# Kernel tuning notes

Measured on AMD Instinct MI355X. Metric: run time of the kernel, lower is better.

Reference implementation:

```python
import jax, jax.numpy as jnp
import numpy as np

B, D, H = 4096, 64, 1024  # batch, state dim, hidden width


def setup_inputs() -> dict:
    key = jax.random.key(0)
    ks = jax.random.split(key, 4)
    def w(k, shape, fan_in):
        return (jax.random.normal(k, shape, jnp.float32) / np.float32(np.sqrt(fan_in)))
    return {
        "x": jax.random.normal(ks[0], (B, 1 + D), jnp.float32),
        "W1": w(ks[1], (D, H), D),
        "b1": jnp.zeros((H,), jnp.float32),
        "W2": w(ks[2], (H, H), H),
        "b2": jnp.zeros((H,), jnp.float32),
        "W3": w(ks[3], (H, D), H),
        "b3": jnp.zeros((D,), jnp.float32),
    }


def _mlp(z, W1, b1, W2, b2, W3, b3):
    # tanh MLP vector field: d -> h -> h -> d
    h = jnp.tanh(z @ W1 + b1)
    h = jnp.tanh(h @ W2 + b2)
    return h @ W3 + b3


def reference(x, W1, b1, W2, b2, W3, b3):
    x_in = x[:, 1:]                        # [B, D] state (col 0 is logp channel)
    f = lambda z: _mlp(z, W1, b1, W2, b2, W3, b3)
    x_out = f(x_in)                        # [B, D]

    # Exact Jacobian trace: same math as the torch per-dim autograd.grad loop,
    # expressed as D forward-mode JVPs vmapped over the identity basis.
    eye = jnp.eye(x_in.shape[1], dtype=x.dtype)

    def diag_entry(e):                     # e: [D] basis vector
        _, t = jax.jvp(f, (x_in,), (jnp.broadcast_to(e, x_in.shape),))
        return t @ e                       # [B] = J[:, i, i]

    trJ = jnp.sum(jax.vmap(diag_entry)(eye), axis=0)  # [B]

    out = jnp.concatenate([-trJ[:, None], x_out], axis=1)  # [B, 1+D]
    return out + 0.0 * x  # faithful to `+ 0 * x` in the original
```

## Files before the change

kernel.cpp:

```cpp
#include <hip/hip_runtime.h>
#include <cmath>

typedef unsigned short u16;
typedef __attribute__((ext_vector_type(8))) short s8v;
typedef __attribute__((ext_vector_type(4))) float f4v;
typedef __attribute__((ext_vector_type(16))) float f16v;

__device__ __forceinline__ u16 f2bf(float f) {
    union { float f; unsigned u; } v; v.f = f;
    unsigned r = v.u + 0x7FFFu + ((v.u >> 16) & 1u);
    return (u16)(r >> 16);
}
__device__ __forceinline__ float tanh_fast(float x) {
    float e = __builtin_amdgcn_exp2f(x * 2.88539008177792681f);
    return 1.f - 2.f * __builtin_amdgcn_rcpf(1.f + e);
}
__device__ __forceinline__ int wslot(int row, int c) {
    return ((((c >> 2) << 6) | ((c & 3) << 4) | (row & 15)) ^ c);
}
__device__ __forceinline__ size_t fragoff(int n, int k) {
    return (((size_t)(n >> 5) * 64 + (k >> 4)) * 64 + (n & 31) + (((k >> 3) & 1) << 5)) * 8 + (k & 7);
}

__launch_bounds__(256)
__global__ void cnf_prep(const float* __restrict__ x, const float* __restrict__ W1,
                         const float* __restrict__ W2, const float* __restrict__ W3,
                         u16* __restrict__ W2Tf, u16* __restrict__ VTf,
                         u16* __restrict__ xb, u16* __restrict__ W1T,
                         u16* __restrict__ W3Tf, float* __restrict__ trJ)
{
    __shared__ float w2s[32][33];
    __shared__ __align__(16) float w1s[64][36];
    const int a = blockIdx.x * 32;
    const int b = blockIdx.y * 32;
    const int t = threadIdx.x;

    #pragma unroll
    for (int it = 0; it < 4; ++it) {
        int idx = t + it * 256;
        w2s[idx >> 5][idx & 31] = W2[(a + (idx >> 5)) * 1024 + b + (idx & 31)];
    }
    #pragma unroll
    for (int it = 0; it < 8; ++it) {
        int idx = t + it * 256;
        w1s[idx >> 5][idx & 31] = W1[(idx >> 5) * 1024 + a + (idx & 31)];
    }
    __syncthreads();

    #pragma unroll
    for (int it = 0; it < 4; ++it) {
        int idx = t + it * 256;
        int rr = idx >> 5, cc = idx & 31;
        W2Tf[fragoff(b + rr, a + cc)] = f2bf(w2s[cc][rr]);
    }
    {
        const int q = t >> 3, pg = t & 7;
        const float* w3row = W3 + (b + q) * 64;
        f4v u = f4v{0.f, 0.f, 0.f, 0.f};
        #pragma unroll
        for (int i4 = 0; i4 < 16; ++i4) {
            f4v w3v = *(const f4v*)&w3row[i4 * 4];
            #pragma unroll
            for (int s = 0; s < 4; ++s) {
                f4v wv = *(const f4v*)&w1s[i4 * 4 + s][pg * 4];
                u += w3v[s] * wv;
            }
        }
        #pragma unroll
        for (int j = 0; j < 4; ++j) {
            const int pp = pg * 4 + j;
            VTf[fragoff(b + q, a + pp)] = f2bf(w2s[pp][q] * u[j]);
        }
    }
    {
        int bid = blockIdx.y * 32 + blockIdx.x;
        int e = bid * 256 + t;
        xb[e] = f2bf(x[(e >> 6) * 65 + 1 + (e & 63)]);
    }
    if (blockIdx.y == 0) {
        int pp = t >> 3, i0 = (t & 7) * 8;
        s8v v;
        #pragma unroll
        for (int j = 0; j < 8; ++j) v[j] = (short)f2bf(w1s[i0 + j][pp]);
        *(s8v*)&W1T[(a + pp) * 64 + i0] = v;
        if (t < 128) trJ[blockIdx.x * 128 + t] = 0.f;
    }
    if (blockIdx.y == 1) {
        int idx = blockIdx.x * 256 + t;
        int n = idx & 63, k0 = (idx >> 6) * 8;
        s8v v;
        #pragma unroll
        for (int j = 0; j < 8; ++j) v[j] = (short)f2bf(W3[(k0 + j) * 64 + n]);
        *(s8v*)&W3Tf[fragoff(n, k0)] = v;
    }
}

__launch_bounds__(256)
__global__ void cnf_gemm1(const u16* __restrict__ xb, const u16* __restrict__ W1T,
                          const float* __restrict__ b1,
                          u16* __restrict__ h1f, u16* __restrict__ g1f)
{
    __shared__ __align__(16) u16 lds[12 * 1024];
    __shared__ __align__(16) u16 hls[128 * 64];
    __shared__ __align__(16) u16 gls[128 * 64];
    const int t = threadIdx.x;
    const int wave = t >> 6, lane = t & 63;
    const int wm = wave >> 1, wn = wave & 1;
    const int g = lane >> 4, lr = lane & 15;
    const int arow0 = blockIdx.x * 128, bcol0 = blockIdx.y * 64;

    #pragma unroll
    for (int i = 0; i < 4; ++i) {
        int ch = t + i * 256, row = ch >> 3, c = ch & 7;
        *(s8v*)&lds[(row >> 4) * 1024 + wslot(row, c) * 8] =
            *(const s8v*)&xb[(arow0 + row) * 64 + c * 8];
    }
    #pragma unroll
    for (int i = 0; i < 2; ++i) {
        int ch = t + i * 256, row = ch >> 3, c = ch & 7;
        *(s8v*)&lds[(8 + (row >> 4)) * 1024 + wslot(row, c) * 8] =
            *(const s8v*)&W1T[(bcol0 + row) * 64 + c * 8];
    }
    __syncthreads();

    f4v acc[4][2];
    #pragma unroll
    for (int mi = 0; mi < 4; ++mi)
        #pragma unroll
        for (int ni = 0; ni < 2; ++ni) acc[mi][ni] = f4v{0.f,0.f,0.f,0.f};

    #pragma unroll
    for (int ks = 0; ks < 2; ++ks) {
        const int lo = (ks * 64 + (lane ^ ((ks * 4 + g) & 7))) * 8;
        s8v af[4], bf[2];
        #pragma unroll
        for (int mi = 0; mi < 4; ++mi) af[mi] = *(const s8v*)&lds[(wm * 4 + mi) * 1024 + lo];
        #pragma unroll
        for (int ni = 0; ni < 2; ++ni) bf[ni] = *(const s8v*)&lds[(8 + wn * 2 + ni) * 1024 + lo];
        #pragma unroll
        for (int mi = 0; mi < 4; ++mi)
            #pragma unroll
            for (int ni = 0; ni < 2; ++ni)
                acc[mi][ni] = __builtin_amdgcn_mfma_f32_16x16x32_bf16(af[mi], bf[ni], acc[mi][ni], 0, 0, 0);
    }

    #pragma unroll
    for (int mi = 0; mi < 4; ++mi) {
        const int rowl = wm * 64 + mi * 16 + g * 4;
        #pragma unroll
        for (int ni = 0; ni < 2; ++ni) {
            const int coll = wn * 32 + ni * 16 + lr;
            const float bv = b1[bcol0 + coll];
            const int cc = coll >> 3, jj = coll & 7;
            #pragma unroll
            for (int r = 0; r < 4; ++r) {
                const int row = rowl + r;
                float h = tanh_fast(acc[mi][ni][r] + bv);
                int idx = row * 64 + ((cc ^ (row & 7)) << 3) + jj;
                hls[idx] = f2bf(h);
                gls[idx] = f2bf(1.f - h * h);
            }
        }
    }
    __syncthreads();

    const int rt0 = arow0 >> 5, kk0 = bcol0 >> 4;
    #pragma unroll
    for (int i = 0; i < 4; ++i) {
        const int tile = (i * 256 + t) >> 6;
        const int ln = t & 63;
        const int rt = tile >> 2, kk = tile & 3;
        const int row = rt * 32 + (ln & 31);
        const int kb = kk * 16 + (ln >> 5) * 8;
        const int src = row * 64 + (((kb >> 3) ^ (row & 7)) << 3);
        const size_t dst = ((size_t)(rt0 + rt) * 64 + (kk0 + kk)) * 512 + ln * 8;
        *(s8v*)&h1f[dst] = *(const s8v*)&hls[src];
        *(s8v*)&g1f[dst] = *(const s8v*)&gls[src];
    }
}

#define LOADB(B, kt)                                                           \
    do { _Pragma("unroll")                                                     \
         for (int _ks = 0; _ks < 2; ++_ks) {                                   \
             size_t _o = (((size_t)(ntb + wn) * 64 + (kt) * 2 + _ks) * 512) + lane * 8; \
             B[_ks*2 + 0] = *(const s8v*)&W2Tf[_o];                            \
             B[_ks*2 + 1] = *(const s8v*)&VTf[_o];                             \
         } } while (0)

#define MIDBODY(kt, AwH, AwG, AlH, AlG, Bc, Bn)                                \
    {                                                                          \
        const u16* _buf = &lds[(kt) & 1][0];                                   \
        s8v a1[2][2], a2[2][2];                                  \
        _Pragma("unroll")                                                      \
        for (int ks = 0; ks < 2; ++ks)                                         \
            _Pragma("unroll")                                                  \
            for (int mt = 0; mt < 2; ++mt) {                                   \
                const int f = ((wrt * 2 + mt) * 2 + ks) * 512 + lane * 8;      \
                a1[ks][mt] = *(const s8v*)&_buf[f];                            \
                a2[ks][mt] = *(const s8v*)&_buf[4096 + f];                     \
            }                                                                  \
        if ((kt) < 30) {                                                       \
            const size_t _go = (size_t)((kt) + 2) * 1024;                      \
            AlH = *(const s8v*)(h1f + sg0 + _go);                              \
            AlG = *(const s8v*)(g1f + sg0 + _go);                              \
        }                                                                      \
        if ((kt) < 31) {                                                       \
            u16* _wb = &lds[((kt) + 1) & 1][0];                                \
            *(s8v*)&_wb[sd0] = AwH; *(s8v*)&_wb[4096 + sd0] = AwG;             \
            LOADB(Bn, (kt) + 1);                                               \
        }                                                                      \
        _Pragma("unroll")                                                      \
        for (int ks = 0; ks < 2; ++ks)                                         \
            _Pragma("unroll")                                                  \
            for (int mt = 0; mt < 2; ++mt) {                                   \
                acc1[mt] = __builtin_amdgcn_mfma_f32_32x32x16_bf16(a1[ks][mt], Bc[ks*2+0], acc1[mt], 0, 0, 0); \
                acc2[mt] = __builtin_amdgcn_mfma_f32_32x32x16_bf16(a2[ks][mt], Bc[ks*2+1], acc2[mt], 0, 0, 0); \
            }                                                                  \
        __syncthreads();                                                       \
    }

__launch_bounds__(512, 1)
__global__ void cnf_mid(const u16* __restrict__ h1f, const u16* __restrict__ g1f,
                        const u16* __restrict__ W2Tf, const u16* __restrict__ VTf,
                        const float* __restrict__ b2,
                        u16* __restrict__ h2f, float* __restrict__ trJ)
{
    __shared__ __align__(16) u16 lds[2][8192];

    const int t = threadIdx.x;
    const int wave = t >> 6, lane = t & 63;
    const int wrt = wave & 1;
    const int wn  = wave >> 1;
    const int bid = blockIdx.x;
    const int k8 = bid & 7, j = bid >> 3;
    const int bx = k8 * 4 + (j & 3);
    const int by = j >> 2;
    const int arow0 = bx * 128;
    const int ntb = by * 4;

    const int lc8 = (t & 63) * 8;
    const int rt_s = t >> 7, kk_s = (t >> 6) & 1;
    const size_t sg0 = ((size_t)(bx * 4 + rt_s) * 64 + kk_s) * 512 + lc8;
    const int sd0 = (rt_s * 2 + kk_s) * 512 + lc8;

    f16v acc1[2], acc2[2];
    #pragma unroll
    for (int mt = 0; mt < 2; ++mt)
        #pragma unroll
        for (int r = 0; r < 16; ++r) { acc1[mt][r] = 0.f; acc2[mt][r] = 0.f; }

    s8v raH, raG, rbH, rbG;
    s8v bA[4], bB[4];

    raH = *(const s8v*)(h1f + sg0);
    raG = *(const s8v*)(g1f + sg0);
    {
        u16* wb = &lds[0][0];
        *(s8v*)&wb[sd0] = raH; *(s8v*)&wb[4096 + sd0] = raG;
    }
    raH = *(const s8v*)(h1f + sg0 + 1024);
    raG = *(const s8v*)(g1f + sg0 + 1024);
    LOADB(bA, 0);
    __syncthreads();

    for (int kt2 = 0; kt2 < 16; ++kt2) {
        const int kt = kt2 * 2;
        MIDBODY(kt,     raH, raG, rbH, rbG, bA, bB);
        MIDBODY(kt + 1, rbH, rbG, raH, raG, bB, bA);
    }

    const int l31 = lane & 31, lh = lane >> 5;
    #pragma unroll
    for (int mt = 0; mt < 2; ++mt) {
        const int rt = (arow0 >> 5) + wrt * 2 + mt;
        const int q0 = (ntb + wn) * 32;
        const float bv = b2[q0 + l31];
        const size_t hb = (((size_t)rt * 64 + ((q0 + l31) >> 4)) * 64
                           + (((l31 >> 3) & 1) << 5)) * 8 + (l31 & 7) + lh * 32;
        float tr[16];
        #pragma unroll
        for (int r = 0; r < 16; ++r) {
            float hh = tanh_fast(acc1[mt][r] + bv);
            float gg = 1.f - hh * hh;
            h2f[hb + ((r & 3) + ((r >> 2) << 3)) * 8] = f2bf(hh);
            tr[r] = acc2[mt][r] * gg;
        }
        #pragma unroll
        for (int off = 1; off < 32; off <<= 1)
            #pragma unroll
            for (int r = 0; r < 16; ++r) tr[r] += __shfl_xor(tr[r], off);
        if (l31 == 0) {
            const int rowb = arow0 + (wrt * 2 + mt) * 32 + lh * 4;
            #pragma unroll
            for (int r = 0; r < 16; ++r)
                atomicAdd(&trJ[rowb + (r & 3) + ((r >> 2) << 3)], tr[r]);
        }
    }
}

__launch_bounds__(256)
__global__ void cnf_out(const u16* __restrict__ h2f, const u16* __restrict__ W3Tf,
                        const float* __restrict__ b3, const float* __restrict__ trJ,
                        float* __restrict__ out)
{
    __shared__ float red[4][32][32];
    const int t = threadIdx.x;
    const int wave = t >> 6, lane = t & 63;
    const int rt = blockIdx.x;
    const int nb = blockIdx.y;

    f16v acc;
    #pragma unroll
    for (int r = 0; r < 16; ++r) acc[r] = 0.f;

    #pragma unroll
    for (int kki = 0; kki < 16; ++kki) {
        const int kk = wave * 16 + kki;
        s8v af = *(const s8v*)&h2f[(((size_t)rt * 64 + kk) * 64 + lane) * 8];
        s8v bf = *(const s8v*)&W3Tf[(((size_t)nb * 64 + kk) * 64 + lane) * 8];
        acc = __builtin_amdgcn_mfma_f32_32x32x16_bf16(af, bf, acc, 0, 0, 0);
    }
    const int l31 = lane & 31, lh = lane >> 5;
    #pragma unroll
    for (int r = 0; r < 16; ++r)
        red[wave][(r & 3) + ((r >> 2) << 3) + lh * 4][l31] = acc[r];
    __syncthreads();

    #pragma unroll
    for (int i = 0; i < 4; ++i) {
        int o = t + i * 256;
        int row = o >> 5, col = o & 31;
        float s = red[0][row][col] + red[1][row][col] + red[2][row][col]
                + red[3][row][col] + b3[nb * 32 + col];
        out[(size_t)(rt * 32 + row) * 65 + 1 + nb * 32 + col] = s;
    }
    if (nb == 0 && t < 32) out[(size_t)(rt * 32 + t) * 65] = -trJ[rt * 32 + t];
}

extern "C" void kernel_launch(void* const* d_in, const int* in_sizes, int n_in,
                              void* d_out, int out_size, void* d_ws, size_t ws_size,
                              hipStream_t stream) {
    const float* x  = (const float*)d_in[0];
    const float* W1 = (const float*)d_in[1];
    const float* b1 = (const float*)d_in[2];
    const float* W2 = (const float*)d_in[3];
    const float* b2 = (const float*)d_in[4];
    const float* W3 = (const float*)d_in[5];
    const float* b3 = (const float*)d_in[6];
    float* out = (float*)d_out;

    char* ws = (char*)d_ws;
    u16*   h1f = (u16*)(ws);
    u16*   g1f = (u16*)(ws + (size_t)( 8u << 20));
    u16*   h2f = (u16*)(ws + (size_t)(16u << 20));
    u16*   W2T = (u16*)(ws + (size_t)(24u << 20));
    u16*   VTb = (u16*)(ws + (size_t)(26u << 20));
    float* trJ = (float*)(ws + (size_t)(28u << 20));
    u16*   xbb = (u16*)(ws + (size_t)(28u << 20) + 65536);
    u16*   W1T = (u16*)(ws + (size_t)(28u << 20) + 65536 + 524288);
    u16*   W3T = (u16*)(ws + (size_t)(28u << 20) + 65536 + 524288 + 131072);

    cnf_prep <<<dim3(32, 32), 256, 0, stream>>>(x, W1, W2, W3, W2T, VTb, xbb, W1T, W3T, trJ);
    cnf_gemm1<<<dim3(32, 16), 256, 0, stream>>>(xbb, W1T, b1, h1f, g1f);
    cnf_mid  <<<256,          512, 0, stream>>>(h1f, g1f, W2T, VTb, b2, h2f, trJ);
    cnf_out  <<<dim3(128, 2), 256, 0, stream>>>(h2f, W3T, b3, trJ, out);
}
```

Measured before the change: 56.77 us.

## Fuse third-layer GEMM into mid kernel via LDS-staged h2 and atomic accumulation

```diff
diff --git a/kernel.cpp b/kernel.cpp
--- a/kernel.cpp
+++ b/kernel.cpp
@@ -27,13 +27,16 @@
                          const float* __restrict__ W2, const float* __restrict__ W3,
                          u16* __restrict__ W2Tf, u16* __restrict__ VTf,
                          u16* __restrict__ xb, u16* __restrict__ W1T,
-                         u16* __restrict__ W3Tf, float* __restrict__ trJ)
+                         u16* __restrict__ W3Tf, float* __restrict__ trJ,
+                         float* __restrict__ obuf)
 {
     __shared__ float w2s[32][33];
     __shared__ __align__(16) float w1s[64][36];
     const int a = blockIdx.x * 32;
     const int b = blockIdx.y * 32;
     const int t = threadIdx.x;
+
+    obuf[(blockIdx.y * 32 + blockIdx.x) * 256 + t] = 0.f;
 
     #pragma unroll
     for (int it = 0; it < 4; ++it) {
@@ -222,8 +225,9 @@
 __launch_bounds__(512, 1)
 __global__ void cnf_mid(const u16* __restrict__ h1f, const u16* __restrict__ g1f,
                         const u16* __restrict__ W2Tf, const u16* __restrict__ VTf,
-                        const float* __restrict__ b2,
-                        u16* __restrict__ h2f, float* __restrict__ trJ)
+                        const u16* __restrict__ W3Tf,
+                        const float* __restrict__ b2, const float* __restrict__ b3,
+                        float* __restrict__ obuf, float* __restrict__ trJ)
 {
     __shared__ __align__(16) u16 lds[2][8192];
 
@@ -231,10 +235,8 @@
     const int wave = t >> 6, lane = t & 63;
     const int wrt = wave & 1;
     const int wn  = wave >> 1;
-    const int bid = blockIdx.x;
-    const int k8 = bid & 7, j = bid >> 3;
-    const int bx = k8 * 4 + (j & 3);
-    const int by = j >> 2;
+    const int bx = blockIdx.x;
+    const int by = blockIdx.y;
     const int arow0 = bx * 128;
     const int ntb = by * 4;
 
@@ -269,20 +271,19 @@
         MIDBODY(kt + 1, rbH, rbG, raH, raG, bB, bA);
     }
 
+    u16* hls = &lds[0][0];
     const int l31 = lane & 31, lh = lane >> 5;
     #pragma unroll
     for (int mt = 0; mt < 2; ++mt) {
-        const int rt = (arow0 >> 5) + wrt * 2 + mt;
-        const int q0 = (ntb + wn) * 32;
-        const float bv = b2[q0 + l31];
-        const size_t hb = (((size_t)rt * 64 + ((q0 + l31) >> 4)) * 64
-                           + (((l31 >> 3) & 1) << 5)) * 8 + (l31 & 7) + lh * 32;
+        const int coll = wn * 32 + l31;
+        const float bv = b2[by * 128 + coll];
         float tr[16];
         #pragma unroll
         for (int r = 0; r < 16; ++r) {
             float hh = tanh_fast(acc1[mt][r] + bv);
             float gg = 1.f - hh * hh;
-            h2f[hb + ((r & 3) + ((r >> 2) << 3)) * 8] = f2bf(hh);
+            const int row = wrt * 64 + mt * 32 + (r & 3) + ((r >> 2) << 3) + lh * 4;
+            hls[row * 128 + (((coll >> 3) ^ (row & 15)) << 3) + (coll & 7)] = f2bf(hh);
             tr[r] = acc2[mt][r] * gg;
         }
         #pragma unroll
@@ -296,45 +297,44 @@
                 atomicAdd(&trJ[rowb + (r & 3) + ((r >> 2) << 3)], tr[r]);
         }
     }
+    __syncthreads();
+
+    {
+        const int ort = wave & 3, ont = wave >> 2;
+        f16v oacc;
+        #pragma unroll
+        for (int r = 0; r < 16; ++r) oacc[r] = 0.f;
+        #pragma unroll
+        for (int kk = 0; kk < 8; ++kk) {
+            const int row = ort * 32 + l31;
+            const int ch = (kk * 2 + lh) ^ (row & 15);
+            s8v af = *(const s8v*)&hls[row * 128 + ch * 8];
+            s8v bf = *(const s8v*)&W3Tf[((size_t)ont * 64 + by * 8 + kk) * 512 + lane * 8];
+            oacc = __builtin_amdgcn_mfma_f32_32x32x16_bf16(af, bf, oacc, 0, 0, 0);
+        }
+        const int col = ont * 32 + l31;
+        const float badd = (by == 0) ? b3[col] : 0.f;
+        #pragma unroll
+        for (int r = 0; r < 16; ++r) {
+            const int row = arow0 + ort * 32 + (r & 3) + ((r >> 2) << 3) + lh * 4;
+            atomicAdd(&obuf[(size_t)row * 64 + col], oacc[r] + badd);
+        }
+    }
 }
 
 __launch_bounds__(256)
-__global__ void cnf_out(const u16* __restrict__ h2f, const u16* __restrict__ W3Tf,
-                        const float* __restrict__ b3, const float* __restrict__ trJ,
+__global__ void cnf_fin(const float* __restrict__ obuf, const float* __restrict__ trJ,
                         float* __restrict__ out)
 {
-    __shared__ float red[4][32][32];
     const int t = threadIdx.x;
-    const int wave = t >> 6, lane = t & 63;
-    const int rt = blockIdx.x;
-    const int nb = blockIdx.y;
-
-    f16v acc;
-    #pragma unroll
-    for (int r = 0; r < 16; ++r) acc[r] = 0.f;
-
-    #pragma unroll
-    for (int kki = 0; kki < 16; ++kki) {
-        const int kk = wave * 16 + kki;
-        s8v af = *(const s8v*)&h2f[(((size_t)rt * 64 + kk) * 64 + lane) * 8];
-        s8v bf = *(const s8v*)&W3Tf[(((size_t)nb * 64 + kk) * 64 + lane) * 8];
-        acc = __builtin_amdgcn_mfma_f32_32x32x16_bf16(af, bf, acc, 0, 0, 0);
-    }
-    const int l31 = lane & 31, lh = lane >> 5;
-    #pragma unroll
-    for (int r = 0; r < 16; ++r)
-        red[wave][(r & 3) + ((r >> 2) << 3) + lh * 4][l31] = acc[r];
-    __syncthreads();
-
+    const int row0 = blockIdx.x * 16;
+    const int c = t & 63, rr = t >> 6;
     #pragma unroll
     for (int i = 0; i < 4; ++i) {
-        int o = t + i * 256;
-        int row = o >> 5, col = o & 31;
-        float s = red[0][row][col] + red[1][row][col] + red[2][row][col]
-                + red[3][row][col] + b3[nb * 32 + col];
-        out[(size_t)(rt * 32 + row) * 65 + 1 + nb * 32 + col] = s;
-    }
-    if (nb == 0 && t < 32) out[(size_t)(rt * 32 + t) * 65] = -trJ[rt * 32 + t];
+        const int row = row0 + rr + i * 4;
+        out[(size_t)row * 65 + 1 + c] = obuf[(size_t)row * 64 + c];
+    }
+    if (t < 16) out[(size_t)(row0 + t) * 65] = -trJ[row0 + t];
 }
 
 extern "C" void kernel_launch(void* const* d_in, const int* in_sizes, int n_in,
@@ -352,7 +352,7 @@
     char* ws = (char*)d_ws;
     u16*   h1f = (u16*)(ws);
     u16*   g1f = (u16*)(ws + (size_t)( 8u << 20));
-    u16*   h2f = (u16*)(ws + (size_t)(16u << 20));
+    float* obf = (float*)(ws + (size_t)(16u << 20));
     u16*   W2T = (u16*)(ws + (size_t)(24u << 20));
     u16*   VTb = (u16*)(ws + (size_t)(26u << 20));
     float* trJ = (float*)(ws + (size_t)(28u << 20));
@@ -360,8 +360,8 @@
     u16*   W1T = (u16*)(ws + (size_t)(28u << 20) + 65536 + 524288);
     u16*   W3T = (u16*)(ws + (size_t)(28u << 20) + 65536 + 524288 + 131072);
 
-    cnf_prep <<<dim3(32, 32), 256, 0, stream>>>(x, W1, W2, W3, W2T, VTb, xbb, W1T, W3T, trJ);
+    cnf_prep <<<dim3(32, 32), 256, 0, stream>>>(x, W1, W2, W3, W2T, VTb, xbb, W1T, W3T, trJ, obf);
     cnf_gemm1<<<dim3(32, 16), 256, 0, stream>>>(xbb, W1T, b1, h1f, g1f);
-    cnf_mid  <<<256,          512, 0, stream>>>(h1f, g1f, W2T, VTb, b2, h2f, trJ);
-    cnf_out  <<<dim3(128, 2), 256, 0, stream>>>(h2f, W3T, b3, trJ, out);
-}
+    cnf_mid  <<<dim3(32, 8),  512, 0, stream>>>(h1f, g1f, W2T, VTb, W3T, b2, b3, obf, trJ);
+    cnf_fin  <<<256,          256, 0, stream>>>(obf, trJ, out);
+}
```

After: 57.82 us. About the same (+1.8%).
